# Kernel tuning notes

Hardware: AMD Instinct MI355X
Metric: run time of the kernel (lower is better)

## Reference

```python
import jax, jax.numpy as jnp
import numpy as np

N_NODES = 100000
N_HEDGES = 20000
N_PAIRS = 1600000
D = 128


def setup_inputs() -> dict:
    key = jax.random.key(0)
    k1, k2, k3, k4, k5 = jax.random.split(key, 5)
    features = jax.random.normal(k1, (N_NODES, D), dtype=jnp.float32)
    W = jax.random.normal(k2, (D, D), dtype=jnp.float32) * (1.0 / np.sqrt(D))
    b = jax.random.normal(k3, (D,), dtype=jnp.float32) * 0.01
    node_idx = jax.random.randint(k4, (N_PAIRS,), 0, N_NODES, dtype=jnp.int32)
    hedge_idx = jax.random.randint(k5, (N_PAIRS,), 0, N_HEDGES, dtype=jnp.int32)
    return {"features": features, "W": W, "b": b,
            "node_idx": node_idx, "hedge_idx": hedge_idx, "n_hedges": N_HEDGES}


def reference(features, W, b, node_idx, hedge_idx, n_hedges):
    # features: [N, D]; (node_idx, hedge_idx): [E] incidence pairs
    N = features.shape[0]
    ones = jnp.ones(node_idx.shape, dtype=features.dtype)
    # node -> hyperedge mean (DGL copy_u + mean over 'in' etype)
    deg_e = jax.ops.segment_sum(ones, hedge_idx, num_segments=n_hedges)  # [He]
    h_edge = jax.ops.segment_sum(features[node_idx], hedge_idx, num_segments=n_hedges)
    h_edge = h_edge / jnp.maximum(deg_e, 1.0)[:, None]  # zero-degree edges -> 0
    # hyperedge -> node mean (copy_u + mean over 'contains' etype)
    deg_n = jax.ops.segment_sum(ones, node_idx, num_segments=N)  # [N]
    h_node = jax.ops.segment_sum(h_edge[hedge_idx], node_idx, num_segments=N)
    h_node = h_node / jnp.maximum(deg_n, 1.0)[:, None]
    # nn.Linear: x @ W.T + b
    return h_node @ W.T + b
```

## Files before the change

kernel.cpp:

```cpp
#include <hip/hip_runtime.h>

static constexpr int kD = 128;
static constexpr int kHedges = 20000;

static constexpr int kNCE = 157;
static constexpr int kCapCE = 11264;
static constexpr int kNCN = 196;
static constexpr int kCapCN = 9216;
static constexpr int kSliceE4 = 1664;
static constexpr int kSliceN4 = 1408;
static constexpr int kPmax = 3200;
static constexpr int kNBmax = 196;

typedef __attribute__((ext_vector_type(8))) short bf16x8;
typedef __attribute__((ext_vector_type(4))) float f32x4;

__device__ __forceinline__ float u2f(unsigned u) { return __uint_as_float(u); }
__device__ __forceinline__ unsigned f2u(float f) { return __float_as_uint(f); }

__device__ __forceinline__ unsigned bfpack(float x, float y) {
  unsigned ux = f2u(x); ux = (ux + 0x7FFFu + ((ux >> 16) & 1u)) >> 16;
  unsigned uy = f2u(y); uy = (uy + 0x7FFFu + ((uy >> 16) & 1u)) & 0xFFFF0000u;
  return ux | uy;
}
__device__ __forceinline__ void bf8_acc(uint4 v, float* a) {
  a[0] += u2f(v.x << 16); a[1] += u2f(v.x & 0xFFFF0000u);
  a[2] += u2f(v.y << 16); a[3] += u2f(v.y & 0xFFFF0000u);
  a[4] += u2f(v.z << 16); a[5] += u2f(v.z & 0xFFFF0000u);
  a[6] += u2f(v.w << 16); a[7] += u2f(v.w & 0xFFFF0000u);
}

__global__ __launch_bounds__(512) void partition_coarse(
    const float* __restrict__ feat, unsigned* __restrict__ feat_bf, int n_feat,
    const float* __restrict__ W, unsigned* __restrict__ Wbf,
    const int* __restrict__ node_idx, const int* __restrict__ hedge_idx,
    int n_pairs, int pgrid,
    int* __restrict__ gcnt_e, int* __restrict__ buf_e,
    int* __restrict__ gcnt_n, int* __restrict__ buf_n) {
  __shared__ unsigned lbuf[kPmax];
  __shared__ int hist[kNBmax], gshift[kNBmax];
  __shared__ int wtot[8];
  const int tid = threadIdx.x;
  {
    const int n8 = n_feat >> 3;
    for (int t = blockIdx.x * 512 + tid; t < n8; t += gridDim.x * 512) {
      long long i = (long long)t * 8;
      const float4 v0 = *(const float4*)(feat + i);
      const float4 v1 = *(const float4*)(feat + i + 4);
      uint4 o;
      o.x = bfpack(v0.x, v0.y); o.y = bfpack(v0.z, v0.w);
      o.z = bfpack(v1.x, v1.y); o.w = bfpack(v1.z, v1.w);
      *(uint4*)(feat_bf + (i >> 1)) = o;
    }
  }
  for (int t = blockIdx.x * 512 + tid; t < kD * 64; t += gridDim.x * 512) {
    int row = t >> 6, m = t & 63;
    Wbf[t] = bfpack(W[row * kD + 2 * m], W[row * kD + 2 * m + 1]);
  }
  const bool isEdge = (blockIdx.x < pgrid);
  const int cchunk = isEdge ? blockIdx.x : blockIdx.x - pgrid;
  const int per_block = (n_pairs + pgrid - 1) / pgrid;
  const int s = cchunk * per_block;
  const int e = min(s + per_block, n_pairs);
  const int cnt = max(e - s, 0);
  const int nb      = isEdge ? kNCE : kNCN;
  const int shift   = isEdge ? 7 : 9;
  const int pshift  = isEdge ? 15 : 17;
  const int* __restrict__ kidx = isEdge ? hedge_idx : node_idx;
  const int* __restrict__ pidx = isEdge ? node_idx : hedge_idx;
  int* __restrict__ gcnt = isEdge ? gcnt_e : gcnt_n;
  int* __restrict__ bufo = isEdge ? buf_e : buf_n;
  const long long capc = isEdge ? kCapCE : kCapCN;
  const unsigned kmask = (1u << pshift) - 1u;
  const int lowmask = (1 << shift) - 1;

  for (int i = tid; i < nb; i += 512) hist[i] = 0;
  __syncthreads();
  for (int i = s + tid; i < e; i += 512) atomicAdd(&hist[kidx[i] >> shift], 1);
  __syncthreads();
  {
    const int lane = tid & 63, wid = tid >> 6;
    int v = (tid < nb) ? hist[tid] : 0;
    int x = v;
#pragma unroll
    for (int d = 1; d < 64; d <<= 1) {
      int y = __shfl_up(x, d, 64);
      if (lane >= d) x += y;
    }
    if (lane == 63) wtot[wid] = x;
    __syncthreads();
    int add = 0;
    for (int w = 0; w < wid; ++w) add += wtot[w];
    if (tid < nb) {
      int lofs = x + add - v;
      int base = (v > 0) ? atomicAdd(&gcnt[tid], v) : 0;
      gshift[tid] = base - lofs;
      hist[tid] = lofs;
    }
  }
  __syncthreads();
  for (int i = s + tid; i < e; i += 512) {
    const unsigned k = (unsigned)kidx[i];
    const unsigned p = (unsigned)pidx[i];
    const int b = (int)(k >> shift);
    const int pos = atomicAdd(&hist[b], 1);
    lbuf[pos] = (p << pshift) | k;
  }
  __syncthreads();
  for (int i = tid; i < cnt; i += 512) {
    const unsigned v = lbuf[i];
    const int k = (int)(v & kmask);
    const int p = (int)(v >> pshift);
    const int b = k >> shift;
    const int pe = gshift[b] + i;
    if (pe < capc) bufo[(long long)b * capc + pe] = (p << shift) | (k & lowmask);
  }
}

__global__ __launch_bounds__(1024) void subsort_kernel(
    int* __restrict__ buf_e, const int* __restrict__ gcnt_e, int* __restrict__ seg_e,
    int* __restrict__ buf_n, const int* __restrict__ gcnt_n, int* __restrict__ seg_n) {
  __shared__ int sbuf[kCapCE];
  __shared__ int bins[513];
  __shared__ int cur[512];
  __shared__ int segs[513];
  __shared__ int wtot[16];
  const int tid = threadIdx.x;
  int nbins, shift, cnt; int* src; int* segout;
  if (blockIdx.x < kNCE) {
    int cb = blockIdx.x; nbins = 128; shift = 7;
    src = buf_e + (long long)cb * kCapCE;
    cnt = min(gcnt_e[cb], kCapCE);
    segout = seg_e + cb * 129;
  } else {
    int cb = blockIdx.x - kNCE; nbins = 512; shift = 9;
    src = buf_n + (long long)cb * kCapCN;
    cnt = min(gcnt_n[cb], kCapCN);
    segout = seg_n + cb * 513;
  }
  const int mask = nbins - 1;
  for (int i = tid; i < nbins; i += 1024) bins[i] = 0;
  __syncthreads();
  for (int i = tid; i < cnt; i += 1024) atomicAdd(&bins[src[i] & mask], 1);
  __syncthreads();
  const int lane = tid & 63, wid = tid >> 6;
  int v = (tid < nbins) ? bins[tid] : 0;
  int x = v;
#pragma unroll
  for (int d = 1; d < 64; d <<= 1) {
    int y = __shfl_up(x, d, 64);
    if (lane >= d) x += y;
  }
  if (lane == 63) wtot[wid] = x;
  __syncthreads();
  int add = 0;
  for (int w = 0; w < wid; ++w) add += wtot[w];
  if (tid < nbins) { segs[tid + 1] = x + add; cur[tid] = x + add - v; }
  if (tid == 0) segs[0] = 0;
  __syncthreads();
  for (int i = tid; i < cnt; i += 1024) {
    int p = src[i];
    int r = atomicAdd(&cur[p & mask], 1);
    sbuf[r] = p >> shift;
  }
  __syncthreads();
  for (int i = tid; i < cnt; i += 1024) src[i] = sbuf[i];
  for (int j = tid; j <= nbins; j += 1024) segout[j] = segs[j];
}

__global__ __launch_bounds__(256) void gather_edge_fused(
    const unsigned* __restrict__ feat_bf, const int* __restrict__ buf_e,
    const int* __restrict__ seg_e, const unsigned* __restrict__ Wbf,
    unsigned* __restrict__ t_edge, int n_hedges) {
  __shared__ int ebuf[kSliceE4];
  __shared__ int segl[17];
  __shared__ unsigned hbf[16][68];
  __shared__ float hout[16][132];
  const int b = blockIdx.x;
  const int tid = threadIdx.x;
  const int h0 = b * 16;
  const int cb = h0 >> 7, j0 = h0 & 127;
  if (tid < 17) segl[tid] = seg_e[cb * 129 + j0 + tid];
  __syncthreads();
  const int sbase = segl[0];
  const int n_sl = min(segl[16] - sbase, kSliceE4);
  const int* src = buf_e + (long long)cb * kCapCE + sbase;
  for (int i = tid; i < n_sl; i += 256) ebuf[i] = src[i];
  __syncthreads();
  const int g = tid >> 4, lane = tid & 15, cw = lane * 4;
  const int gh = h0 + g;
  float a[8] = {}, a2[8] = {};
  int deg = 0;
  if (gh < n_hedges) {
    deg = segl[g + 1] - segl[g];
    const int s0 = min(segl[g] - sbase, n_sl);
    const int e0 = min(segl[g + 1] - sbase, n_sl);
    int j = s0;
    const int jend8 = s0 + ((e0 - s0) & ~7);
    if (j < jend8) {
      uint4 A0 = *(const uint4*)(feat_bf + (long long)ebuf[j] * 64 + cw);
      uint4 A1 = *(const uint4*)(feat_bf + (long long)ebuf[j + 1] * 64 + cw);
      uint4 A2 = *(const uint4*)(feat_bf + (long long)ebuf[j + 2] * 64 + cw);
      uint4 A3 = *(const uint4*)(feat_bf + (long long)ebuf[j + 3] * 64 + cw);
      uint4 A4 = *(const uint4*)(feat_bf + (long long)ebuf[j + 4] * 64 + cw);
      uint4 A5 = *(const uint4*)(feat_bf + (long long)ebuf[j + 5] * 64 + cw);
      uint4 A6 = *(const uint4*)(feat_bf + (long long)ebuf[j + 6] * 64 + cw);
      uint4 A7 = *(const uint4*)(feat_bf + (long long)ebuf[j + 7] * 64 + cw);
      j += 8;
      for (; j < jend8; j += 8) {
        uint4 B0 = *(const uint4*)(feat_bf + (long long)ebuf[j] * 64 + cw);
        uint4 B1 = *(const uint4*)(feat_bf + (long long)ebuf[j + 1] * 64 + cw);
        uint4 B2 = *(const uint4*)(feat_bf + (long long)ebuf[j + 2] * 64 + cw);
        uint4 B3 = *(const uint4*)(feat_bf + (long long)ebuf[j + 3] * 64 + cw);
        uint4 B4 = *(const uint4*)(feat_bf + (long long)ebuf[j + 4] * 64 + cw);
        uint4 B5 = *(const uint4*)(feat_bf + (long long)ebuf[j + 5] * 64 + cw);
        uint4 B6 = *(const uint4*)(feat_bf + (long long)ebuf[j + 6] * 64 + cw);
        uint4 B7 = *(const uint4*)(feat_bf + (long long)ebuf[j + 7] * 64 + cw);
        bf8_acc(A0, a); bf8_acc(A1, a2); bf8_acc(A2, a); bf8_acc(A3, a2);
        bf8_acc(A4, a); bf8_acc(A5, a2); bf8_acc(A6, a); bf8_acc(A7, a2);
        A0 = B0; A1 = B1; A2 = B2; A3 = B3;
        A4 = B4; A5 = B5; A6 = B6; A7 = B7;
      }
      bf8_acc(A0, a); bf8_acc(A1, a2); bf8_acc(A2, a); bf8_acc(A3, a2);
      bf8_acc(A4, a); bf8_acc(A5, a2); bf8_acc(A6, a); bf8_acc(A7, a2);
    }
    for (; j < e0; ++j) {
      uint4 v = *(const uint4*)(feat_bf + (long long)ebuf[j] * 64 + cw);
      bf8_acc(v, a);
    }
  }
  {
    const float inv = 1.0f / fmaxf((float)deg, 1.0f);
    uint4 o;
    o.x = bfpack((a[0] + a2[0]) * inv, (a[1] + a2[1]) * inv);
    o.y = bfpack((a[2] + a2[2]) * inv, (a[3] + a2[3]) * inv);
    o.z = bfpack((a[4] + a2[4]) * inv, (a[5] + a2[5]) * inv);
    o.w = bfpack((a[6] + a2[6]) * inv, (a[7] + a2[7]) * inv);
    *(uint4*)(&hbf[g][cw]) = o;
  }
  __syncthreads();
  {
    const int wv = tid >> 6;
    const int l = tid & 63;
    const int frow = l & 15;
    const int kgrp = l >> 4;
    f32x4 acc0 = {0.f, 0.f, 0.f, 0.f}, acc1 = {0.f, 0.f, 0.f, 0.f};
#pragma unroll
    for (int kk = 0; kk < 4; ++kk) {
      const int wofs = kk * 16 + kgrp * 4;
      bf16x8 af = *(const bf16x8*)(&hbf[frow][wofs]);
      bf16x8 bf0 = *(const bf16x8*)(Wbf + ((2 * wv) * 16 + frow) * 64 + wofs);
      bf16x8 bf1 = *(const bf16x8*)(Wbf + ((2 * wv + 1) * 16 + frow) * 64 + wofs);
      acc0 = __builtin_amdgcn_mfma_f32_16x16x32_bf16(af, bf0, acc0, 0, 0, 0);
      acc1 = __builtin_amdgcn_mfma_f32_16x16x32_bf16(af, bf1, acc1, 0, 0, 0);
    }
#pragma unroll
    for (int r = 0; r < 4; ++r) {
      hout[kgrp * 4 + r][(2 * wv) * 16 + frow] = acc0[r];
      hout[kgrp * 4 + r][(2 * wv + 1) * 16 + frow] = acc1[r];
    }
  }
  __syncthreads();
  if (gh < n_hedges) {
    const float* hr = &hout[g][lane * 8];
    uint4 o;
    o.x = bfpack(hr[0], hr[1]);
    o.y = bfpack(hr[2], hr[3]);
    o.z = bfpack(hr[4], hr[5]);
    o.w = bfpack(hr[6], hr[7]);
    *(uint4*)(t_edge + (long long)gh * 64 + cw) = o;
  }
}

__global__ __launch_bounds__(256) void gather_node_v4(
    const unsigned* __restrict__ t_edge, const int* __restrict__ buf_n,
    const int* __restrict__ seg_n, const float* __restrict__ bias,
    float* __restrict__ out, int n_nodes) {
  __shared__ int ebuf[kSliceN4];
  __shared__ int segl[65];
  const int b = blockIdx.x;
  const int tid = threadIdx.x;
  const int n0 = b * 64;
  const int cb = n0 >> 9, j0 = n0 & 511;
  if (tid < 65) segl[tid] = seg_n[cb * 513 + j0 + tid];
  __syncthreads();
  const int sbase = segl[0];
  const int n_sl = min(segl[64] - sbase, kSliceN4);
  const int* src = buf_n + (long long)cb * kCapCN + sbase;
  for (int i = tid; i < n_sl; i += 256) ebuf[i] = src[i];
  __syncthreads();
  const int g = tid >> 4, lane = tid & 15, cw = lane * 4;
  const float4 b0 = *(const float4*)(bias + lane * 8);
  const float4 b1 = *(const float4*)(bias + lane * 8 + 4);
  for (int nl = g; nl < 64; nl += 16) {
    int gn = n0 + nl;
    if (gn >= n_nodes) continue;
    const int deg = segl[nl + 1] - segl[nl];
    const int s0 = min(segl[nl] - sbase, n_sl);
    const int e0 = min(segl[nl + 1] - sbase, n_sl);
    float a[8] = {}, a2[8] = {};
    int j = s0;
    const int jend8 = s0 + ((e0 - s0) & ~7);
    if (j < jend8) {
      uint4 A0 = *(const uint4*)(t_edge + (long long)ebuf[j] * 64 + cw);
      uint4 A1 = *(const uint4*)(t_edge + (long long)ebuf[j + 1] * 64 + cw);
      uint4 A2 = *(const uint4*)(t_edge + (long long)ebuf[j + 2] * 64 + cw);
      uint4 A3 = *(const uint4*)(t_edge + (long long)ebuf[j + 3] * 64 + cw);
      uint4 A4 = *(const uint4*)(t_edge + (long long)ebuf[j + 4] * 64 + cw);
      uint4 A5 = *(const uint4*)(t_edge + (long long)ebuf[j + 5] * 64 + cw);
      uint4 A6 = *(const uint4*)(t_edge + (long long)ebuf[j + 6] * 64 + cw);
      uint4 A7 = *(const uint4*)(t_edge + (long long)ebuf[j + 7] * 64 + cw);
      j += 8;
      for (; j < jend8; j += 8) {
        uint4 B0 = *(const uint4*)(t_edge + (long long)ebuf[j] * 64 + cw);
        uint4 B1 = *(const uint4*)(t_edge + (long long)ebuf[j + 1] * 64 + cw);
        uint4 B2 = *(const uint4*)(t_edge + (long long)ebuf[j + 2] * 64 + cw);
        uint4 B3 = *(const uint4*)(t_edge + (long long)ebuf[j + 3] * 64 + cw);
        uint4 B4 = *(const uint4*)(t_edge + (long long)ebuf[j + 4] * 64 + cw);
        uint4 B5 = *(const uint4*)(t_edge + (long long)ebuf[j + 5] * 64 + cw);
        uint4 B6 = *(const uint4*)(t_edge + (long long)ebuf[j + 6] * 64 + cw);
        uint4 B7 = *(const uint4*)(t_edge + (long long)ebuf[j + 7] * 64 + cw);
        bf8_acc(A0, a); bf8_acc(A1, a2); bf8_acc(A2, a); bf8_acc(A3, a2);
        bf8_acc(A4, a); bf8_acc(A5, a2); bf8_acc(A6, a); bf8_acc(A7, a2);
        A0 = B0; A1 = B1; A2 = B2; A3 = B3;
        A4 = B4; A5 = B5; A6 = B6; A7 = B7;
      }
      bf8_acc(A0, a); bf8_acc(A1, a2); bf8_acc(A2, a); bf8_acc(A3, a2);
      bf8_acc(A4, a); bf8_acc(A5, a2); bf8_acc(A6, a); bf8_acc(A7, a2);
    }
    for (; j < e0; ++j) {
      uint4 v = *(const uint4*)(t_edge + (long long)ebuf[j] * 64 + cw);
      bf8_acc(v, a);
    }
#pragma unroll
    for (int t = 0; t < 8; ++t) a[t] += a2[t];
    float inv = 1.0f / fmaxf((float)deg, 1.0f);
    float4 o0, o1;
    o0.x = fmaf(a[0], inv, b0.x); o0.y = fmaf(a[1], inv, b0.y);
    o0.z = fmaf(a[2], inv, b0.z); o0.w = fmaf(a[3], inv, b0.w);
    o1.x = fmaf(a[4], inv, b1.x); o1.y = fmaf(a[5], inv, b1.y);
    o1.z = fmaf(a[6], inv, b1.z); o1.w = fmaf(a[7], inv, b1.w);
    float* op = out + (long long)gn * kD + lane * 8;
    *(float4*)op = o0;
    *(float4*)(op + 4) = o1;
  }
}

extern "C" void kernel_launch(void* const* d_in, const int* in_sizes, int n_in,
                              void* d_out, int out_size, void* d_ws, size_t ws_size,
                              hipStream_t stream) {
  const float* feat      = (const float*)d_in[0];
  const float* W         = (const float*)d_in[1];
  const float* b         = (const float*)d_in[2];
  const int*   node_idx  = (const int*)d_in[3];
  const int*   hedge_idx = (const int*)d_in[4];

  const int n_pairs  = in_sizes[3];
  const int n_nodes  = in_sizes[0] / kD;
  const int n_hedges = kHedges;
  const int n_feat   = in_sizes[0];

  unsigned* feat_bf = (unsigned*)d_out;

  const int n_rows_pad = ((n_hedges + 63) / 64) * 64;
  unsigned* t_edge = (unsigned*)d_ws;
  int* buf_e = (int*)(t_edge + (size_t)n_rows_pad * 64);
  int* buf_n = buf_e + (size_t)kNCE * kCapCE;
  int* seg_e = buf_n + (size_t)kNCN * kCapCN;
  int* seg_n = seg_e + (size_t)kNCE * 129;
  int* gcnt_e = seg_n + (size_t)kNCN * 513;
  int* gcnt_n = gcnt_e + kNCE;
  unsigned* Wbf = (unsigned*)(gcnt_n + kNCN);

  hipMemsetAsync(gcnt_e, 0, (size_t)(kNCE + kNCN) * sizeof(int), stream);

  int pgrid = (n_pairs + kPmax - 1) / kPmax;
  if (pgrid < 512) pgrid = 512;

  partition_coarse<<<2 * pgrid, 512, 0, stream>>>(
      feat, feat_bf, n_feat, W, Wbf,
      node_idx, hedge_idx, n_pairs, pgrid, gcnt_e, buf_e, gcnt_n, buf_n);

  subsort_kernel<<<kNCE + kNCN, 1024, 0, stream>>>(
      buf_e, gcnt_e, seg_e, buf_n, gcnt_n, seg_n);

  gather_edge_fused<<<(n_hedges + 15) / 16, 256, 0, stream>>>(
      feat_bf, buf_e, seg_e, Wbf, t_edge, n_hedges);

  gather_node_v4<<<(n_nodes + 63) / 64, 256, 0, stream>>>(
      t_edge, buf_n, seg_n, b, (float*)d_out, n_nodes);
}
```

Before: 250.8 us.

## Split subsort and overlap node-bucket sort with edge gather kernel

Node-side coarse buckets are halved in size (256 nodes per bucket, 391 buckets) so each fits in a 256-thread block's shared memory. The node subsort moves out of the combined subsort kernel into extra blocks of the edge-gather kernel, sharing LDS through a union, so it runs alongside the edge gather instead of in a separate serial phase. The edge subsort becomes its own specialized kernel. The trade-off is more partition histogram bins and larger per-block LDS in the gather kernel, which may lower its occupancy.

```diff
diff --git a/kernel.cpp b/kernel.cpp
--- a/kernel.cpp
+++ b/kernel.cpp
@@ -5,12 +5,12 @@
 
 static constexpr int kNCE = 157;
 static constexpr int kCapCE = 11264;
-static constexpr int kNCN = 196;
-static constexpr int kCapCN = 9216;
+static constexpr int kNCN = 391;
+static constexpr int kCapCN = 4608;
 static constexpr int kSliceE4 = 1664;
 static constexpr int kSliceN4 = 1408;
 static constexpr int kPmax = 3200;
-static constexpr int kNBmax = 196;
+static constexpr int kNBmax = 391;
 
 typedef __attribute__((ext_vector_type(8))) short bf16x8;
 typedef __attribute__((ext_vector_type(4))) float f32x4;
@@ -64,7 +64,7 @@
   const int e = min(s + per_block, n_pairs);
   const int cnt = max(e - s, 0);
   const int nb      = isEdge ? kNCE : kNCN;
-  const int shift   = isEdge ? 7 : 9;
+  const int shift   = isEdge ? 7 : 8;
   const int pshift  = isEdge ? 15 : 17;
   const int* __restrict__ kidx = isEdge ? hedge_idx : node_idx;
   const int* __restrict__ pidx = isEdge ? node_idx : hedge_idx;
@@ -117,34 +117,24 @@
   }
 }
 
-__global__ __launch_bounds__(1024) void subsort_kernel(
-    int* __restrict__ buf_e, const int* __restrict__ gcnt_e, int* __restrict__ seg_e,
-    int* __restrict__ buf_n, const int* __restrict__ gcnt_n, int* __restrict__ seg_n) {
+__global__ __launch_bounds__(1024) void subsort_edge(
+    int* __restrict__ buf_e, const int* __restrict__ gcnt_e, int* __restrict__ seg_e) {
   __shared__ int sbuf[kCapCE];
-  __shared__ int bins[513];
-  __shared__ int cur[512];
-  __shared__ int segs[513];
+  __shared__ int bins[129];
+  __shared__ int cur[128];
+  __shared__ int segs[129];
   __shared__ int wtot[16];
   const int tid = threadIdx.x;
-  int nbins, shift, cnt; int* src; int* segout;
-  if (blockIdx.x < kNCE) {
-    int cb = blockIdx.x; nbins = 128; shift = 7;
-    src = buf_e + (long long)cb * kCapCE;
-    cnt = min(gcnt_e[cb], kCapCE);
-    segout = seg_e + cb * 129;
-  } else {
-    int cb = blockIdx.x - kNCE; nbins = 512; shift = 9;
-    src = buf_n + (long long)cb * kCapCN;
-    cnt = min(gcnt_n[cb], kCapCN);
-    segout = seg_n + cb * 513;
-  }
-  const int mask = nbins - 1;
-  for (int i = tid; i < nbins; i += 1024) bins[i] = 0;
-  __syncthreads();
-  for (int i = tid; i < cnt; i += 1024) atomicAdd(&bins[src[i] & mask], 1);
+  const int cb = blockIdx.x;
+  int* src = buf_e + (long long)cb * kCapCE;
+  const int cnt = min(gcnt_e[cb], kCapCE);
+  int* segout = seg_e + cb * 129;
+  if (tid < 128) bins[tid] = 0;
+  __syncthreads();
+  for (int i = tid; i < cnt; i += 1024) atomicAdd(&bins[src[i] & 127], 1);
   __syncthreads();
   const int lane = tid & 63, wid = tid >> 6;
-  int v = (tid < nbins) ? bins[tid] : 0;
+  int v = (tid < 128) ? bins[tid] : 0;
   int x = v;
 #pragma unroll
   for (int d = 1; d < 64; d <<= 1) {
@@ -155,67 +145,116 @@
   __syncthreads();
   int add = 0;
   for (int w = 0; w < wid; ++w) add += wtot[w];
-  if (tid < nbins) { segs[tid + 1] = x + add; cur[tid] = x + add - v; }
+  if (tid < 128) { segs[tid + 1] = x + add; cur[tid] = x + add - v; }
   if (tid == 0) segs[0] = 0;
   __syncthreads();
   for (int i = tid; i < cnt; i += 1024) {
     int p = src[i];
-    int r = atomicAdd(&cur[p & mask], 1);
-    sbuf[r] = p >> shift;
+    int r = atomicAdd(&cur[p & 127], 1);
+    sbuf[r] = p >> 7;
   }
   __syncthreads();
   for (int i = tid; i < cnt; i += 1024) src[i] = sbuf[i];
-  for (int j = tid; j <= nbins; j += 1024) segout[j] = segs[j];
-}
-
-__global__ __launch_bounds__(256) void gather_edge_fused(
+  if (tid <= 128) segout[tid] = segs[tid];
+}
+
+struct ShmGather {
+  float hout[16][132];
+  unsigned hbf[16][68];
+  int ebuf[kSliceE4];
+  int segl[17];
+};
+struct ShmSort {
+  int sbuf[kCapCN];
+  int bins[257];
+  int cur[256];
+  int segs[257];
+  int wtot[4];
+};
+union __align__(16) ShmU { ShmGather g; ShmSort s; };
+
+__global__ __launch_bounds__(256) void gather_edge_sortn(
     const unsigned* __restrict__ feat_bf, const int* __restrict__ buf_e,
     const int* __restrict__ seg_e, const unsigned* __restrict__ Wbf,
-    unsigned* __restrict__ t_edge, int n_hedges) {
-  __shared__ int ebuf[kSliceE4];
-  __shared__ int segl[17];
-  __shared__ unsigned hbf[16][68];
-  __shared__ float hout[16][132];
-  const int b = blockIdx.x;
+    unsigned* __restrict__ t_edge, int n_hedges,
+    int* __restrict__ buf_n, const int* __restrict__ gcnt_n,
+    int* __restrict__ seg_n) {
+  __shared__ ShmU sh;
   const int tid = threadIdx.x;
+  if (blockIdx.x < kNCN) {
+    const int cb = blockIdx.x;
+    int* src = buf_n + (long long)cb * kCapCN;
+    const int cnt = min(gcnt_n[cb], kCapCN);
+    int* segout = seg_n + cb * 257;
+    sh.s.bins[tid] = 0;
+    __syncthreads();
+    for (int i = tid; i < cnt; i += 256) atomicAdd(&sh.s.bins[src[i] & 255], 1);
+    __syncthreads();
+    const int lane = tid & 63, wid = tid >> 6;
+    int v = sh.s.bins[tid];
+    int x = v;
+#pragma unroll
+    for (int d = 1; d < 64; d <<= 1) {
+      int y = __shfl_up(x, d, 64);
+      if (lane >= d) x += y;
+    }
+    if (lane == 63) sh.s.wtot[wid] = x;
+    __syncthreads();
+    int add = 0;
+    for (int w = 0; w < wid; ++w) add += sh.s.wtot[w];
+    sh.s.segs[tid + 1] = x + add;
+    sh.s.cur[tid] = x + add - v;
+    if (tid == 0) sh.s.segs[0] = 0;
+    __syncthreads();
+    for (int i = tid; i < cnt; i += 256) {
+      int p = src[i];
+      int r = atomicAdd(&sh.s.cur[p & 255], 1);
+      sh.s.sbuf[r] = p >> 8;
+    }
+    __syncthreads();
+    for (int i = tid; i < cnt; i += 256) src[i] = sh.s.sbuf[i];
+    for (int j = tid; j <= 256; j += 256) segout[j] = sh.s.segs[j];
+    return;
+  }
+  const int b = blockIdx.x - kNCN;
   const int h0 = b * 16;
   const int cb = h0 >> 7, j0 = h0 & 127;
-  if (tid < 17) segl[tid] = seg_e[cb * 129 + j0 + tid];
-  __syncthreads();
-  const int sbase = segl[0];
-  const int n_sl = min(segl[16] - sbase, kSliceE4);
+  if (tid < 17) sh.g.segl[tid] = seg_e[cb * 129 + j0 + tid];
+  __syncthreads();
+  const int sbase = sh.g.segl[0];
+  const int n_sl = min(sh.g.segl[16] - sbase, kSliceE4);
   const int* src = buf_e + (long long)cb * kCapCE + sbase;
-  for (int i = tid; i < n_sl; i += 256) ebuf[i] = src[i];
+  for (int i = tid; i < n_sl; i += 256) sh.g.ebuf[i] = src[i];
   __syncthreads();
   const int g = tid >> 4, lane = tid & 15, cw = lane * 4;
   const int gh = h0 + g;
   float a[8] = {}, a2[8] = {};
   int deg = 0;
   if (gh < n_hedges) {
-    deg = segl[g + 1] - segl[g];
-    const int s0 = min(segl[g] - sbase, n_sl);
-    const int e0 = min(segl[g + 1] - sbase, n_sl);
+    deg = sh.g.segl[g + 1] - sh.g.segl[g];
+    const int s0 = min(sh.g.segl[g] - sbase, n_sl);
+    const int e0 = min(sh.g.segl[g + 1] - sbase, n_sl);
     int j = s0;
     const int jend8 = s0 + ((e0 - s0) & ~7);
     if (j < jend8) {
-      uint4 A0 = *(const uint4*)(feat_bf + (long long)ebuf[j] * 64 + cw);
-      uint4 A1 = *(const uint4*)(feat_bf + (long long)ebuf[j + 1] * 64 + cw);
-      uint4 A2 = *(const uint4*)(feat_bf + (long long)ebuf[j + 2] * 64 + cw);
-      uint4 A3 = *(const uint4*)(feat_bf + (long long)ebuf[j + 3] * 64 + cw);
-      uint4 A4 = *(const uint4*)(feat_bf + (long long)ebuf[j + 4] * 64 + cw);
-      uint4 A5 = *(const uint4*)(feat_bf + (long long)ebuf[j + 5] * 64 + cw);
-      uint4 A6 = *(const uint4*)(feat_bf + (long long)ebuf[j + 6] * 64 + cw);
-      uint4 A7 = *(const uint4*)(feat_bf + (long long)ebuf[j + 7] * 64 + cw);
+      uint4 A0 = *(const uint4*)(feat_bf + (long long)sh.g.ebuf[j] * 64 + cw);
+      uint4 A1 = *(const uint4*)(feat_bf + (long long)sh.g.ebuf[j + 1] * 64 + cw);
+      uint4 A2 = *(const uint4*)(feat_bf + (long long)sh.g.ebuf[j + 2] * 64 + cw);
+      uint4 A3 = *(const uint4*)(feat_bf + (long long)sh.g.ebuf[j + 3] * 64 + cw);
+      uint4 A4 = *(const uint4*)(feat_bf + (long long)sh.g.ebuf[j + 4] * 64 + cw);
+      uint4 A5 = *(const uint4*)(feat_bf + (long long)sh.g.ebuf[j + 5] * 64 + cw);
+      uint4 A6 = *(const uint4*)(feat_bf + (long long)sh.g.ebuf[j + 6] * 64 + cw);
+      uint4 A7 = *(const uint4*)(feat_bf + (long long)sh.g.ebuf[j + 7] * 64 + cw);
       j += 8;
       for (; j < jend8; j += 8) {
-        uint4 B0 = *(const uint4*)(feat_bf + (long long)ebuf[j] * 64 + cw);
-        uint4 B1 = *(const uint4*)(feat_bf + (long long)ebuf[j + 1] * 64 + cw);
-        uint4 B2 = *(const uint4*)(feat_bf + (long long)ebuf[j + 2] * 64 + cw);
-        uint4 B3 = *(const uint4*)(feat_bf + (long long)ebuf[j + 3] * 64 + cw);
-        uint4 B4 = *(const uint4*)(feat_bf + (long long)ebuf[j + 4] * 64 + cw);
-        uint4 B5 = *(const uint4*)(feat_bf + (long long)ebuf[j + 5] * 64 + cw);
-        uint4 B6 = *(const uint4*)(feat_bf + (long long)ebuf[j + 6] * 64 + cw);
-        uint4 B7 = *(const uint4*)(feat_bf + (long long)ebuf[j + 7] * 64 + cw);
+        uint4 B0 = *(const uint4*)(feat_bf + (long long)sh.g.ebuf[j] * 64 + cw);
+        uint4 B1 = *(const uint4*)(feat_bf + (long long)sh.g.ebuf[j + 1] * 64 + cw);
+        uint4 B2 = *(const uint4*)(feat_bf + (long long)sh.g.ebuf[j + 2] * 64 + cw);
+        uint4 B3 = *(const uint4*)(feat_bf + (long long)sh.g.ebuf[j + 3] * 64 + cw);
+        uint4 B4 = *(const uint4*)(feat_bf + (long long)sh.g.ebuf[j + 4] * 64 + cw);
+        uint4 B5 = *(const uint4*)(feat_bf + (long long)sh.g.ebuf[j + 5] * 64 + cw);
+        uint4 B6 = *(const uint4*)(feat_bf + (long long)sh.g.ebuf[j + 6] * 64 + cw);
+        uint4 B7 = *(const uint4*)(feat_bf + (long long)sh.g.ebuf[j + 7] * 64 + cw);
         bf8_acc(A0, a); bf8_acc(A1, a2); bf8_acc(A2, a); bf8_acc(A3, a2);
         bf8_acc(A4, a); bf8_acc(A5, a2); bf8_acc(A6, a); bf8_acc(A7, a2);
         A0 = B0; A1 = B1; A2 = B2; A3 = B3;
@@ -225,7 +264,7 @@
       bf8_acc(A4, a); bf8_acc(A5, a2); bf8_acc(A6, a); bf8_acc(A7, a2);
     }
     for (; j < e0; ++j) {
-      uint4 v = *(const uint4*)(feat_bf + (long long)ebuf[j] * 64 + cw);
+      uint4 v = *(const uint4*)(feat_bf + (long long)sh.g.ebuf[j] * 64 + cw);
       bf8_acc(v, a);
     }
   }
@@ -236,7 +275,7 @@
     o.y = bfpack((a[2] + a2[2]) * inv, (a[3] + a2[3]) * inv);
     o.z = bfpack((a[4] + a2[4]) * inv, (a[5] + a2[5]) * inv);
     o.w = bfpack((a[6] + a2[6]) * inv, (a[7] + a2[7]) * inv);
-    *(uint4*)(&hbf[g][cw]) = o;
+    *(uint4*)(&sh.g.hbf[g][cw]) = o;
   }
   __syncthreads();
   {
@@ -248,7 +287,7 @@
 #pragma unroll
     for (int kk = 0; kk < 4; ++kk) {
       const int wofs = kk * 16 + kgrp * 4;
-      bf16x8 af = *(const bf16x8*)(&hbf[frow][wofs]);
+      bf16x8 af = *(const bf16x8*)(&sh.g.hbf[frow][wofs]);
       bf16x8 bf0 = *(const bf16x8*)(Wbf + ((2 * wv) * 16 + frow) * 64 + wofs);
       bf16x8 bf1 = *(const bf16x8*)(Wbf + ((2 * wv + 1) * 16 + frow) * 64 + wofs);
       acc0 = __builtin_amdgcn_mfma_f32_16x16x32_bf16(af, bf0, acc0, 0, 0, 0);
@@ -256,13 +295,13 @@
     }
 #pragma unroll
     for (int r = 0; r < 4; ++r) {
-      hout[kgrp * 4 + r][(2 * wv) * 16 + frow] = acc0[r];
-      hout[kgrp * 4 + r][(2 * wv + 1) * 16 + frow] = acc1[r];
+      sh.g.hout[kgrp * 4 + r][(2 * wv) * 16 + frow] = acc0[r];
+      sh.g.hout[kgrp * 4 + r][(2 * wv + 1) * 16 + frow] = acc1[r];
     }
   }
   __syncthreads();
   if (gh < n_hedges) {
-    const float* hr = &hout[g][lane * 8];
+    const float* hr = &sh.g.hout[g][lane * 8];
     uint4 o;
     o.x = bfpack(hr[0], hr[1]);
     o.y = bfpack(hr[2], hr[3]);
@@ -281,8 +320,8 @@
   const int b = blockIdx.x;
   const int tid = threadIdx.x;
   const int n0 = b * 64;
-  const int cb = n0 >> 9, j0 = n0 & 511;
-  if (tid < 65) segl[tid] = seg_n[cb * 513 + j0 + tid];
+  const int cb = n0 >> 8, j0 = n0 & 255;
+  if (tid < 65) segl[tid] = seg_n[cb * 257 + j0 + tid];
   __syncthreads();
   const int sbase = segl[0];
   const int n_sl = min(segl[64] - sbase, kSliceN4);
@@ -368,7 +407,7 @@
   int* buf_n = buf_e + (size_t)kNCE * kCapCE;
   int* seg_e = buf_n + (size_t)kNCN * kCapCN;
   int* seg_n = seg_e + (size_t)kNCE * 129;
-  int* gcnt_e = seg_n + (size_t)kNCN * 513;
+  int* gcnt_e = seg_n + (size_t)kNCN * 257;
   int* gcnt_n = gcnt_e + kNCE;
   unsigned* Wbf = (unsigned*)(gcnt_n + kNCN);
 
@@ -381,11 +420,11 @@
       feat, feat_bf, n_feat, W, Wbf,
       node_idx, hedge_idx, n_pairs, pgrid, gcnt_e, buf_e, gcnt_n, buf_n);
 
-  subsort_kernel<<<kNCE + kNCN, 1024, 0, stream>>>(
-      buf_e, gcnt_e, seg_e, buf_n, gcnt_n, seg_n);
-
-  gather_edge_fused<<<(n_hedges + 15) / 16, 256, 0, stream>>>(
-      feat_bf, buf_e, seg_e, Wbf, t_edge, n_hedges);
+  subsort_edge<<<kNCE, 1024, 0, stream>>>(buf_e, gcnt_e, seg_e);
+
+  gather_edge_sortn<<<kNCN + (n_hedges + 15) / 16, 256, 0, stream>>>(
+      feat_bf, buf_e, seg_e, Wbf, t_edge, n_hedges,
+      buf_n, gcnt_n, seg_n);
 
   gather_node_v4<<<(n_nodes + 63) / 64, 256, 0, stream>>>(
       t_edge, buf_n, seg_n, b, (float*)d_out, n_nodes);
```

After: 252.9 us. About the same (+0.8%).
